# Kernel optimization log

Hardware: AMD Instinct MI355X
Metric: run time of the kernel (lower is better)

Reference implementation:

```python
import jax, jax.numpy as jnp
import numpy as np

TEMPERATURE = 0.07
EPS = 1e-8


def _cosine_sim(a, b):
    # F.cosine_similarity(a[:,None], b[None,:], dim=-1) as a normalized matmul
    an = a / jnp.maximum(jnp.linalg.norm(a, axis=-1, keepdims=True), EPS)
    bn = b / jnp.maximum(jnp.linalg.norm(b, axis=-1, keepdims=True), EPS)
    return an @ bn.T  # [N, M]


def setup_inputs() -> dict:
    key = jax.random.key(0)
    k1, k2, k3, k4 = jax.random.split(key, 4)
    B, M, D, C = 512, 65536, 256, 10
    return {
        "q": jax.random.normal(k1, (B, D), dtype=jnp.float32),
        "labels": jax.random.randint(k2, (B,), 0, C, dtype=jnp.int64),
        "pro_memory": jax.random.normal(k3, (M, D), dtype=jnp.float32),
        "pro_labels": jax.random.randint(k4, (M,), 0, C, dtype=jnp.int64),
    }


def reference(q, labels, pro_memory, pro_labels):
    B = q.shape[0]
    # --- memory branch (adapt_to='prototype'), memory detached ---
    memory_logits = _cosine_sim(q, jax.lax.stop_gradient(pro_memory)) / TEMPERATURE  # [B, M]
    memory_targets = (labels[:, None] == pro_labels[None, :]).astype(jnp.float32)

    # --- source (in-batch) branch; second q is detached in matrix_sim ---
    src_contrast = _cosine_sim(q, jax.lax.stop_gradient(q)) / TEMPERATURE  # [B, B]
    src_max = jax.lax.stop_gradient(jnp.max(src_contrast, axis=1, keepdims=True))
    src_logits = src_contrast - src_max
    src_mask = 1.0 - jnp.eye(B, dtype=jnp.float32)  # zero the diagonal (self)
    src_targets = (labels[:, None] == labels[None, :]).astype(jnp.float32) * src_mask

    targets = jnp.concatenate([src_targets, memory_targets], axis=1)     # [B, B+M]
    logits = jnp.concatenate([src_logits, memory_logits], axis=1)        # [B, B+M]
    exp_logits = jnp.concatenate(
        [jnp.exp(src_logits) * src_mask, jnp.exp(memory_logits)], axis=1
    )
    log_prob = logits - jnp.log(exp_logits.sum(axis=1, keepdims=True))
    mean_log_prob_pos = (targets * log_prob).sum(axis=1) / targets.sum(axis=1)
    return -jnp.mean(mean_log_prob_pos)
```

## Files before the change

kernel.cpp:

```cpp
#include <hip/hip_runtime.h>
#include <stdint.h>
#include <math.h>

#define B_N 512
#define M_N 65536
#define D_N 256
#define C_N 10
#define TEMP_INV 14.285714285714286f
#define LOG2E_F 1.4426950408889634f
#define K2C (LOG2E_F * TEMP_INV)

typedef __attribute__((ext_vector_type(8))) __bf16 bf16x8;
typedef __attribute__((ext_vector_type(4))) float f32x4;

__device__ __forceinline__ unsigned short f2bf(float f) {
  unsigned int u = __float_as_uint(f);
  return (unsigned short)((u + 0x7FFFu + ((u >> 16) & 1u)) >> 16);
}
__device__ __forceinline__ float bf2f(unsigned short s) {
  return __uint_as_float(((unsigned int)s) << 16);
}

__global__ __launch_bounds__(256) void k_norm_full(const float* __restrict__ pm,
                                                   const float* __restrict__ q,
                                                   unsigned short* __restrict__ pnb,
                                                   float* __restrict__ qn,
                                                   unsigned short* __restrict__ qnb,
                                                   unsigned short* __restrict__ qnbF,
                                                   float* __restrict__ P,
                                                   int* __restrict__ cnt,
                                                   float* __restrict__ Zt,
                                                   float* __restrict__ Ss,
                                                   float* __restrict__ ns_,
                                                   float* __restrict__ out) {
  const int tid = threadIdx.x, w = tid >> 6, l = tid & 63;
  const int g = l >> 4, qs = l & 15;
  if (blockIdx.x == 0) {
    for (int i = tid; i < C_N * D_N; i += 256) P[i] = 0.f;
    if (tid < C_N) cnt[tid] = 0;
    for (int i = tid; i < B_N; i += 256) { Zt[i] = 0.f; Ss[i] = 0.f; ns_[i] = 0.f; }
    if (tid == 0) out[0] = 0.f;
  }
  if (blockIdx.x < 2048) {
    const int rbase = blockIdx.x * 32 + w * 8;
#pragma unroll
    for (int it = 0; it < 2; ++it) {
      const int r = rbase + it * 4 + g;
      const float* src = pm + (size_t)r * D_N;
      float4 v[4];
#pragma unroll
      for (int c = 0; c < 4; ++c) v[c] = *(const float4*)(src + qs * 4 + c * 64);
      float ss = 0.f;
#pragma unroll
      for (int c = 0; c < 4; ++c)
        ss += v[c].x * v[c].x + v[c].y * v[c].y + v[c].z * v[c].z + v[c].w * v[c].w;
      ss += __shfl_xor(ss, 1, 64);
      ss += __shfl_xor(ss, 2, 64);
      ss += __shfl_xor(ss, 4, 64);
      ss += __shfl_xor(ss, 8, 64);
      const float rv = 1.0f / fmaxf(sqrtf(ss), 1e-8f);
      unsigned short* dst = pnb + (size_t)r * D_N;
#pragma unroll
      for (int c = 0; c < 4; ++c) {
        ushort4 o;
        o.x = f2bf(v[c].x * rv); o.y = f2bf(v[c].y * rv);
        o.z = f2bf(v[c].z * rv); o.w = f2bf(v[c].w * rv);
        *(ushort4*)(dst + qs * 4 + c * 64) = o;
      }
    }
  } else {
    const int r = (blockIdx.x - 2048) * 16 + w * 4 + g;
    const float* src = q + (size_t)r * D_N;
    float4 v[4];
#pragma unroll
    for (int c = 0; c < 4; ++c) v[c] = *(const float4*)(src + qs * 4 + c * 64);
    float ss = 0.f;
#pragma unroll
    for (int c = 0; c < 4; ++c)
      ss += v[c].x * v[c].x + v[c].y * v[c].y + v[c].z * v[c].z + v[c].w * v[c].w;
    ss += __shfl_xor(ss, 1, 64);
    ss += __shfl_xor(ss, 2, 64);
    ss += __shfl_xor(ss, 4, 64);
    ss += __shfl_xor(ss, 8, 64);
    const float rv = 1.0f / fmaxf(sqrtf(ss), 1e-8f);
    float* dstf = qn + (size_t)r * D_N;
    unsigned short* dstb = qnb + (size_t)r * D_N;
#pragma unroll
    for (int c = 0; c < 4; ++c) {
      float4 o4;
      o4.x = v[c].x * rv; o4.y = v[c].y * rv; o4.z = v[c].z * rv; o4.w = v[c].w * rv;
      *(float4*)(dstf + qs * 4 + c * 64) = o4;
      ushort4 o;
      o.x = f2bf(o4.x); o.y = f2bf(o4.y); o.z = f2bf(o4.z); o.w = f2bf(o4.w);
      *(ushort4*)(dstb + qs * 4 + c * 64) = o;
      const int kc = (qs >> 1) + c * 8;
      *(ushort4*)(qnbF + (((size_t)kc * 512 + r) << 3) + (qs & 1) * 4) = o;
    }
  }
}

__global__ __launch_bounds__(256, 4) void k_mega(const unsigned short* __restrict__ qnb,
                                                 const unsigned short* __restrict__ qnbF,
                                                 const unsigned short* __restrict__ pnb,
                                                 const int* __restrict__ labels,
                                                 const int* __restrict__ pl,
                                                 float* __restrict__ Zt,
                                                 float* __restrict__ Ss,
                                                 float* __restrict__ ns_,
                                                 float* __restrict__ Zpart,
                                                 float* __restrict__ part) {
  __shared__ __align__(16) unsigned char smem[40960];
  const int bid = blockIdx.x;
  const int tid = threadIdx.x, w = tid >> 6, lane = tid & 63;
  const int rsel = lane & 15, hi = lane >> 4;

  if (bid < 1024) {
    unsigned short* Bs = (unsigned short*)smem;
    float* zall = (float*)(smem + 34816);
    const unsigned short* Bb = pnb + (size_t)bid * 64 * D_N;
    {
      bf16x8 t8[8];
#pragma unroll
      for (int i = 0; i < 8; ++i) {
        const int c = i * 256 + tid;
        t8[i] = *(const bf16x8*)(Bb + (size_t)c * 8);
      }
#pragma unroll
      for (int i = 0; i < 8; ++i) {
        const int c = i * 256 + tid;
        const int r = c >> 5, s = c & 31;
        *(bf16x8*)((char*)Bs + r * 544 + s * 16) = t8[i];
      }
    }
    __syncthreads();

#pragma unroll
    for (int bt = 0; bt < 2; ++bt) {
      f32x4 acc[4][4];
#pragma unroll
      for (int mi = 0; mi < 4; ++mi)
#pragma unroll
        for (int ni = 0; ni < 4; ++ni)
          acc[mi][ni] = (f32x4){0.f, 0.f, 0.f, 0.f};
#pragma unroll
      for (int it = 0; it < 8; ++it) {
        const int kc = it * 4 + hi;
        bf16x8 af[4], bfr[4];
#pragma unroll
        for (int mi = 0; mi < 4; ++mi) {
          const int r = bt * 256 + w * 64 + mi * 16 + rsel;
          af[mi] = *(const bf16x8*)(qnbF + (((size_t)kc * 512 + r) << 3));
        }
#pragma unroll
        for (int ni = 0; ni < 4; ++ni) {
          const int rB = ni * 16 + rsel;
          bfr[ni] = *(const bf16x8*)((const char*)Bs + rB * 544 + kc * 16);
        }
#pragma unroll
        for (int mi = 0; mi < 4; ++mi)
#pragma unroll
          for (int ni = 0; ni < 4; ++ni)
            acc[mi][ni] = __builtin_amdgcn_mfma_f32_16x16x32_bf16(af[mi], bfr[ni], acc[mi][ni], 0, 0, 0);
      }
#pragma unroll
      for (int mi = 0; mi < 4; ++mi) {
        float sv[4] = {0.f, 0.f, 0.f, 0.f};
#pragma unroll
        for (int ni = 0; ni < 4; ++ni)
#pragma unroll
          for (int rg = 0; rg < 4; ++rg)
            sv[rg] += __builtin_amdgcn_exp2f(acc[mi][ni][rg] * K2C);
#pragma unroll
        for (int rg = 0; rg < 4; ++rg) {
          float v = sv[rg];
          v += __shfl_xor(v, 1, 64);
          v += __shfl_xor(v, 2, 64);
          v += __shfl_xor(v, 4, 64);
          v += __shfl_xor(v, 8, 64);
          if (rsel == 0)
            zall[bt * 256 + w * 64 + mi * 16 + hi * 4 + rg] = v;
        }
      }
    }
    __syncthreads();
    float* zp = Zpart + (size_t)bid * 512;
    for (int i = tid; i < 512; i += 256) zp[i] = zall[i];
  } else if (bid < 1040) {
    unsigned short* As = (unsigned short*)smem;
    unsigned short* Bs = (unsigned short*)(smem + 16384);
    int* labR = (int*)(smem + 32768);
    int* labJ = (int*)(smem + 33280);
    float* zr = (float*)(smem + 33792);
    float* sr = (float*)(smem + 34304);
    float* nr = (float*)(smem + 34816);
    const int sb_id = bid - 1024;
    const int bt = sb_id >> 2, jt = sb_id & 3;
    const unsigned short* Ab = qnb + (size_t)(bt * 128) * D_N;
    const unsigned short* Bb = qnb + (size_t)(jt * 128) * D_N;
    if (tid < 128) {
      labR[tid] = labels[bt * 128 + tid];
      labJ[tid] = labels[jt * 128 + tid];
      zr[tid] = 0.f; sr[tid] = 0.f; nr[tid] = 0.f;
    }
    f32x4 acc[4][4];
#pragma unroll
    for (int mi = 0; mi < 4; ++mi)
#pragma unroll
      for (int ni = 0; ni < 4; ++ni)
        acc[mi][ni] = (f32x4){0.f, 0.f, 0.f, 0.f};
    const int wr = w >> 1, wc = w & 1;
    for (int ks = 0; ks < 4; ++ks) {
      const int kk = ks * 64;
#pragma unroll
      for (int i = 0; i < 4; ++i) {
        const int cbase = i * 256 + w * 64;
        const int c = cbase + lane;
        const int r = c >> 3;
        const int ss2 = (c & 7) ^ (r & 7);
        __builtin_amdgcn_global_load_lds(
            (const __attribute__((address_space(1))) void*)(Ab + (size_t)r * D_N + kk + ss2 * 8),
            (__attribute__((address_space(3))) void*)(As + cbase * 8), 16, 0, 0);
        __builtin_amdgcn_global_load_lds(
            (const __attribute__((address_space(1))) void*)(Bb + (size_t)r * D_N + kk + ss2 * 8),
            (__attribute__((address_space(3))) void*)(Bs + cbase * 8), 16, 0, 0);
      }
      __syncthreads();
#pragma unroll
      for (int ksl = 0; ksl < 2; ++ksl) {
        const int sb = ksl * 4 + hi;
        bf16x8 af[4], bfr[4];
#pragma unroll
        for (int mi = 0; mi < 4; ++mi) {
          const int r = wr * 64 + mi * 16 + rsel;
          af[mi] = *(const bf16x8*)((const char*)As + r * 128 + ((sb ^ (r & 7)) * 16));
        }
#pragma unroll
        for (int ni = 0; ni < 4; ++ni) {
          const int r = wc * 64 + ni * 16 + rsel;
          bfr[ni] = *(const bf16x8*)((const char*)Bs + r * 128 + ((sb ^ (r & 7)) * 16));
        }
#pragma unroll
        for (int mi = 0; mi < 4; ++mi)
#pragma unroll
          for (int ni = 0; ni < 4; ++ni)
            acc[mi][ni] = __builtin_amdgcn_mfma_f32_16x16x32_bf16(af[mi], bfr[ni], acc[mi][ni], 0, 0, 0);
      }
      __syncthreads();
    }
#pragma unroll
    for (int mi = 0; mi < 4; ++mi) {
      float zs[4] = {0.f, 0.f, 0.f, 0.f};
      float sv[4] = {0.f, 0.f, 0.f, 0.f};
      float nv[4] = {0.f, 0.f, 0.f, 0.f};
#pragma unroll
      for (int ni = 0; ni < 4; ++ni) {
        const int j_loc = wc * 64 + ni * 16 + rsel;
        const int jg = jt * 128 + j_loc;
        const int lj = labJ[j_loc];
#pragma unroll
        for (int rg_ = 0; rg_ < 4; ++rg_) {
          const int r_loc = wr * 64 + mi * 16 + hi * 4 + rg_;
          const int rg = bt * 128 + r_loc;
          const float lg = acc[mi][ni][rg_] * TEMP_INV - TEMP_INV;
          if (rg != jg) {
            zs[rg_] += __builtin_amdgcn_exp2f(lg * LOG2E_F);
            if (labR[r_loc] == lj) { sv[rg_] += lg; nv[rg_] += 1.f; }
          }
        }
      }
#pragma unroll
      for (int rg_ = 0; rg_ < 4; ++rg_) {
        float z = zs[rg_], s = sv[rg_], n = nv[rg_];
        z += __shfl_xor(z, 1, 64); z += __shfl_xor(z, 2, 64);
        z += __shfl_xor(z, 4, 64); z += __shfl_xor(z, 8, 64);
        s += __shfl_xor(s, 1, 64); s += __shfl_xor(s, 2, 64);
        s += __shfl_xor(s, 4, 64); s += __shfl_xor(s, 8, 64);
        n += __shfl_xor(n, 1, 64); n += __shfl_xor(n, 2, 64);
        n += __shfl_xor(n, 4, 64); n += __shfl_xor(n, 8, 64);
        if (rsel == 0) {
          const int r_loc = wr * 64 + mi * 16 + hi * 4 + rg_;
          atomicAdd(&zr[r_loc], z);
          atomicAdd(&sr[r_loc], s);
          atomicAdd(&nr[r_loc], n);
        }
      }
    }
    __syncthreads();
    if (tid < 128) {
      atomicAdd(&Zt[bt * 128 + tid], zr[tid]);
      atomicAdd(&Ss[bt * 128 + tid], sr[tid]);
      atomicAdd(&ns_[bt * 128 + tid], nr[tid]);
    }
  } else {
    const int cb = bid - 1040;
    const int rbase = cb * 128;
    float4 a0 = {0,0,0,0}, a1 = {0,0,0,0}, a2 = {0,0,0,0}, a3 = {0,0,0,0}, a4 = {0,0,0,0};
    float4 a5 = {0,0,0,0}, a6 = {0,0,0,0}, a7 = {0,0,0,0}, a8 = {0,0,0,0}, a9 = {0,0,0,0};
    for (int j = 0; j < 32; ++j) {
      const int row = rbase + j * 4 + w;
      const ushort4 u = *(const ushort4*)(pnb + (size_t)row * D_N + lane * 4);
      float4 v;
      v.x = bf2f(u.x); v.y = bf2f(u.y); v.z = bf2f(u.z); v.w = bf2f(u.w);
      const int cls = pl[row];
      switch (cls) {
        case 0: a0.x += v.x; a0.y += v.y; a0.z += v.z; a0.w += v.w; break;
        case 1: a1.x += v.x; a1.y += v.y; a1.z += v.z; a1.w += v.w; break;
        case 2: a2.x += v.x; a2.y += v.y; a2.z += v.z; a2.w += v.w; break;
        case 3: a3.x += v.x; a3.y += v.y; a3.z += v.z; a3.w += v.w; break;
        case 4: a4.x += v.x; a4.y += v.y; a4.z += v.z; a4.w += v.w; break;
        case 5: a5.x += v.x; a5.y += v.y; a5.z += v.z; a5.w += v.w; break;
        case 6: a6.x += v.x; a6.y += v.y; a6.z += v.z; a6.w += v.w; break;
        case 7: a7.x += v.x; a7.y += v.y; a7.z += v.z; a7.w += v.w; break;
        case 8: a8.x += v.x; a8.y += v.y; a8.z += v.z; a8.w += v.w; break;
        default: a9.x += v.x; a9.y += v.y; a9.z += v.z; a9.w += v.w; break;
      }
    }
    float* Pl = (float*)smem;
#define WRCLS(k, ak) *(float4*)(Pl + ((w * 10 + (k)) * 256 + lane * 4)) = ak;
    WRCLS(0, a0) WRCLS(1, a1) WRCLS(2, a2) WRCLS(3, a3) WRCLS(4, a4)
    WRCLS(5, a5) WRCLS(6, a6) WRCLS(7, a7) WRCLS(8, a8) WRCLS(9, a9)
#undef WRCLS
    __syncthreads();
    float* dst = part + (size_t)cb * (C_N * D_N);
    for (int i = tid; i < C_N * D_N; i += 256)
      dst[i] = Pl[i] + Pl[2560 + i] + Pl[5120 + i] + Pl[7680 + i];
  }
}

__global__ __launch_bounds__(256) void k_reduce2(const float* __restrict__ part,
                                                 const int* __restrict__ pl,
                                                 const float* __restrict__ Zpart,
                                                 float* __restrict__ P,
                                                 int* __restrict__ cnt,
                                                 float* __restrict__ Zt) {
  const int tid = threadIdx.x, w = tid >> 6, lane = tid & 63;
  if (blockIdx.x < 40) {
    __shared__ int xs[4];
    const int c = blockIdx.x >> 2, q = blockIdx.x & 3;
    float s = 0.f;
#pragma unroll 8
    for (int i = 0; i < 128; ++i)
      s += part[(size_t)(q * 128 + i) * (C_N * D_N) + c * 256 + tid];
    atomicAdd(&P[c * 256 + tid], s);
    int x = 0;
    const int* plq = pl + q * 16384;
#pragma unroll 8
    for (int jj = 0; jj < 64; ++jj)
      x += (plq[jj * 256 + tid] == c) ? 1 : 0;
    x += __shfl_xor(x, 32, 64);
    x += __shfl_xor(x, 16, 64);
    x += __shfl_xor(x, 8, 64);
    x += __shfl_xor(x, 4, 64);
    x += __shfl_xor(x, 2, 64);
    x += __shfl_xor(x, 1, 64);
    if (lane == 0) xs[w] = x;
    __syncthreads();
    if (tid == 0) atomicAdd(&cnt[c], xs[0] + xs[1] + xs[2] + xs[3]);
  } else {
    __shared__ float zl[4][64];
    const int zb = blockIdx.x - 40;
    const int b = zb * 64 + (tid & 63);
    const int s = tid >> 6;
    float acc = 0.f;
#pragma unroll 8
    for (int k = 0; k < 256; ++k)
      acc += Zpart[(size_t)(s * 256 + k) * 512 + b];
    zl[s][tid & 63] = acc;
    __syncthreads();
    if (tid < 64)
      Zt[zb * 64 + tid] += zl[0][tid] + zl[1][tid] + zl[2][tid] + zl[3][tid];
  }
}

__global__ __launch_bounds__(256) void k_final(const float* __restrict__ qn,
                                               const int* __restrict__ labels,
                                               const float* __restrict__ P,
                                               const int* __restrict__ cnt,
                                               const float* __restrict__ Zt,
                                               const float* __restrict__ Ss,
                                               const float* __restrict__ ns_,
                                               float* __restrict__ out) {
  __shared__ float partl[4];
  const int tid = threadIdx.x, w = tid >> 6, lane = tid & 63;
  const int b = blockIdx.x * 4 + w;
  const int cls = labels[b];
  const float4 v = *(const float4*)(qn + (size_t)b * D_N + lane * 4);
  const float4 p = *(const float4*)(P + (size_t)cls * D_N + lane * 4);
  float d = v.x * p.x + v.y * p.y + v.z * p.z + v.w * p.w;
  d += __shfl_xor(d, 32, 64);
  d += __shfl_xor(d, 16, 64);
  d += __shfl_xor(d, 8, 64);
  d += __shfl_xor(d, 4, 64);
  d += __shfl_xor(d, 2, 64);
  d += __shfl_xor(d, 1, 64);
  if (lane == 0) {
    const float smem_ = d * TEMP_INV;
    const float ntot = ns_[b] + (float)cnt[cls];
    partl[w] = (Ss[b] + smem_) / ntot - logf(Zt[b]);
  }
  __syncthreads();
  if (tid == 0)
    atomicAdd(out, -(partl[0] + partl[1] + partl[2] + partl[3]) * (1.0f / (float)B_N));
}

extern "C" void kernel_launch(void* const* d_in, const int* in_sizes, int n_in,
                              void* d_out, int out_size, void* d_ws, size_t ws_size,
                              hipStream_t stream) {
  const float* q = (const float*)d_in[0];
  const int* labels = (const int*)d_in[1];
  const float* pm = (const float*)d_in[2];
  const int* pl = (const int*)d_in[3];
  float* out = (float*)d_out;

  char* wsb = (char*)d_ws;
  unsigned short* pnb = (unsigned short*)wsb;
  float* qn = (float*)(wsb + 33554432);
  unsigned short* qnb = (unsigned short*)(wsb + 34078720);
  float* P = (float*)(wsb + 34340864);
  int* cnt = (int*)(wsb + 34351104);
  float* Zt = (float*)(wsb + 34351168);
  float* Ss = (float*)(wsb + 34353216);
  float* ns_ = (float*)(wsb + 34355264);
  float* part = (float*)(wsb + 34357312);
  float* Zpart = (float*)(wsb + 39620672);
  unsigned short* qnbF = (unsigned short*)(wsb + 41717824);

  k_norm_full<<<2080, 256, 0, stream>>>(pm, q, pnb, qn, qnb, qnbF, P, cnt, Zt, Ss, ns_, out);
  k_mega<<<1552, 256, 0, stream>>>(qnb, qnbF, pnb, labels, pl, Zt, Ss, ns_, Zpart, part);
  k_reduce2<<<48, 256, 0, stream>>>(part, pl, Zpart, P, cnt, Zt);
  k_final<<<128, 256, 0, stream>>>(qn, labels, P, cnt, Zt, Ss, ns_, out);
}
```

Measured before the change: 81.08 us.

## Fuse per-class prototype sums into GEMM blocks and retile q fragment layout

The separate 512 class-sum blocks are removed. Each GEMM block now computes per-class column sums from the prototype tile it already holds in shared memory, which avoids re-reading the prototype bank from global memory. The q fragment buffer is reordered so the four k-chunks a lane group needs within one iteration sit next to each other, which should improve load coalescing. The costs are double the partial-sum buffer (1024 rows reduced instead of 512) and a lowered occupancy hint from 4 to 3 blocks, which may change register allocation.

New measurement: 96.87 us. 19.5% more time.

```diff
diff --git a/kernel.cpp b/kernel.cpp
--- a/kernel.cpp
+++ b/kernel.cpp
@@ -94,12 +94,13 @@
       o.x = f2bf(o4.x); o.y = f2bf(o4.y); o.z = f2bf(o4.z); o.w = f2bf(o4.w);
       *(ushort4*)(dstb + qs * 4 + c * 64) = o;
       const int kc = (qs >> 1) + c * 8;
-      *(ushort4*)(qnbF + (((size_t)kc * 512 + r) << 3) + (qs & 1) * 4) = o;
+      const int itc = kc >> 2, hic = kc & 3;
+      *(ushort4*)(qnbF + ((((size_t)itc * 512 + r) * 4 + hic) << 3) + (qs & 1) * 4) = o;
     }
   }
 }
 
-__global__ __launch_bounds__(256, 4) void k_mega(const unsigned short* __restrict__ qnb,
+__global__ __launch_bounds__(256, 3) void k_mega(const unsigned short* __restrict__ qnb,
                                                  const unsigned short* __restrict__ qnbF,
                                                  const unsigned short* __restrict__ pnb,
                                                  const int* __restrict__ labels,
@@ -109,7 +110,7 @@
                                                  float* __restrict__ ns_,
                                                  float* __restrict__ Zpart,
                                                  float* __restrict__ part) {
-  __shared__ __align__(16) unsigned char smem[40960];
+  __shared__ __align__(16) unsigned char smem[37120];
   const int bid = blockIdx.x;
   const int tid = threadIdx.x, w = tid >> 6, lane = tid & 63;
   const int rsel = lane & 15, hi = lane >> 4;
@@ -117,7 +118,9 @@
   if (bid < 1024) {
     unsigned short* Bs = (unsigned short*)smem;
     float* zall = (float*)(smem + 34816);
+    int* plL = (int*)(smem + 36864);
     const unsigned short* Bb = pnb + (size_t)bid * 64 * D_N;
+    if (tid < 64) plL[tid] = pl[bid * 64 + tid];
     {
       bf16x8 t8[8];
 #pragma unroll
@@ -149,7 +152,7 @@
 #pragma unroll
         for (int mi = 0; mi < 4; ++mi) {
           const int r = bt * 256 + w * 64 + mi * 16 + rsel;
-          af[mi] = *(const bf16x8*)(qnbF + (((size_t)kc * 512 + r) << 3));
+          af[mi] = *(const bf16x8*)(qnbF + ((((size_t)it * 512 + r) * 4 + hi) << 3));
         }
 #pragma unroll
         for (int ni = 0; ni < 4; ++ni) {
@@ -185,7 +188,31 @@
     __syncthreads();
     float* zp = Zpart + (size_t)bid * 512;
     for (int i = tid; i < 512; i += 256) zp[i] = zall[i];
-  } else if (bid < 1040) {
+
+    {
+      float s0 = 0.f, s1 = 0.f, s2 = 0.f, s3 = 0.f, s4 = 0.f;
+      float s5 = 0.f, s6 = 0.f, s7 = 0.f, s8 = 0.f, s9 = 0.f;
+#pragma unroll 8
+      for (int r = 0; r < 64; ++r) {
+        const float v = bf2f(*(const unsigned short*)((const char*)Bs + r * 544 + tid * 2));
+        switch (plL[r]) {
+          case 0: s0 += v; break;
+          case 1: s1 += v; break;
+          case 2: s2 += v; break;
+          case 3: s3 += v; break;
+          case 4: s4 += v; break;
+          case 5: s5 += v; break;
+          case 6: s6 += v; break;
+          case 7: s7 += v; break;
+          case 8: s8 += v; break;
+          default: s9 += v; break;
+        }
+      }
+      float* dst = part + (size_t)bid * (C_N * D_N) + tid;
+      dst[0] = s0; dst[256] = s1; dst[512] = s2; dst[768] = s3; dst[1024] = s4;
+      dst[1280] = s5; dst[1536] = s6; dst[1792] = s7; dst[2048] = s8; dst[2304] = s9;
+    }
+  } else {
     unsigned short* As = (unsigned short*)smem;
     unsigned short* Bs = (unsigned short*)(smem + 16384);
     int* labR = (int*)(smem + 32768);
@@ -291,39 +318,6 @@
       atomicAdd(&Ss[bt * 128 + tid], sr[tid]);
       atomicAdd(&ns_[bt * 128 + tid], nr[tid]);
     }
-  } else {
-    const int cb = bid - 1040;
-    const int rbase = cb * 128;
-    float4 a0 = {0,0,0,0}, a1 = {0,0,0,0}, a2 = {0,0,0,0}, a3 = {0,0,0,0}, a4 = {0,0,0,0};
-    float4 a5 = {0,0,0,0}, a6 = {0,0,0,0}, a7 = {0,0,0,0}, a8 = {0,0,0,0}, a9 = {0,0,0,0};
-    for (int j = 0; j < 32; ++j) {
-      const int row = rbase + j * 4 + w;
-      const ushort4 u = *(const ushort4*)(pnb + (size_t)row * D_N + lane * 4);
-      float4 v;
-      v.x = bf2f(u.x); v.y = bf2f(u.y); v.z = bf2f(u.z); v.w = bf2f(u.w);
-      const int cls = pl[row];
-      switch (cls) {
-        case 0: a0.x += v.x; a0.y += v.y; a0.z += v.z; a0.w += v.w; break;
-        case 1: a1.x += v.x; a1.y += v.y; a1.z += v.z; a1.w += v.w; break;
-        case 2: a2.x += v.x; a2.y += v.y; a2.z += v.z; a2.w += v.w; break;
-        case 3: a3.x += v.x; a3.y += v.y; a3.z += v.z; a3.w += v.w; break;
-        case 4: a4.x += v.x; a4.y += v.y; a4.z += v.z; a4.w += v.w; break;
-        case 5: a5.x += v.x; a5.y += v.y; a5.z += v.z; a5.w += v.w; break;
-        case 6: a6.x += v.x; a6.y += v.y; a6.z += v.z; a6.w += v.w; break;
-        case 7: a7.x += v.x; a7.y += v.y; a7.z += v.z; a7.w += v.w; break;
-        case 8: a8.x += v.x; a8.y += v.y; a8.z += v.z; a8.w += v.w; break;
-        default: a9.x += v.x; a9.y += v.y; a9.z += v.z; a9.w += v.w; break;
-      }
-    }
-    float* Pl = (float*)smem;
-#define WRCLS(k, ak) *(float4*)(Pl + ((w * 10 + (k)) * 256 + lane * 4)) = ak;
-    WRCLS(0, a0) WRCLS(1, a1) WRCLS(2, a2) WRCLS(3, a3) WRCLS(4, a4)
-    WRCLS(5, a5) WRCLS(6, a6) WRCLS(7, a7) WRCLS(8, a8) WRCLS(9, a9)
-#undef WRCLS
-    __syncthreads();
-    float* dst = part + (size_t)cb * (C_N * D_N);
-    for (int i = tid; i < C_N * D_N; i += 256)
-      dst[i] = Pl[i] + Pl[2560 + i] + Pl[5120 + i] + Pl[7680 + i];
   }
 }
 
@@ -339,8 +333,8 @@
     const int c = blockIdx.x >> 2, q = blockIdx.x & 3;
     float s = 0.f;
 #pragma unroll 8
-    for (int i = 0; i < 128; ++i)
-      s += part[(size_t)(q * 128 + i) * (C_N * D_N) + c * 256 + tid];
+    for (int i = 0; i < 256; ++i)
+      s += part[(size_t)(q * 256 + i) * (C_N * D_N) + c * 256 + tid];
     atomicAdd(&P[c * 256 + tid], s);
     int x = 0;
     const int* plq = pl + q * 16384;
@@ -422,11 +416,11 @@
   float* Ss = (float*)(wsb + 34353216);
   float* ns_ = (float*)(wsb + 34355264);
   float* part = (float*)(wsb + 34357312);
-  float* Zpart = (float*)(wsb + 39620672);
-  unsigned short* qnbF = (unsigned short*)(wsb + 41717824);
+  float* Zpart = (float*)(wsb + 44843072);
+  unsigned short* qnbF = (unsigned short*)(wsb + 46940224);
 
   k_norm_full<<<2080, 256, 0, stream>>>(pm, q, pnb, qn, qnb, qnbF, P, cnt, Zt, Ss, ns_, out);
-  k_mega<<<1552, 256, 0, stream>>>(qnb, qnbF, pnb, labels, pl, Zt, Ss, ns_, Zpart, part);
+  k_mega<<<1040, 256, 0, stream>>>(qnb, qnbF, pnb, labels, pl, Zt, Ss, ns_, Zpart, part);
   k_reduce2<<<48, 256, 0, stream>>>(part, pl, Zpart, P, cnt, Zt);
   k_final<<<128, 256, 0, stream>>>(qn, labels, P, cnt, Zt, Ss, ns_, out);
 }
```

## Split class-sum work into its own kernel and retile GEMM with 512-thread blocks

Applied to the files above, without the earlier changes.

Moves the per-class prototype accumulation out of the mega kernel into a separate k_class launch. The GEMM kernel now uses 512-thread blocks with 8 waves per 64-row memory tile. Each wave preloads all 16 A fragments for its 32 query rows into registers before the MFMA loop, instead of reloading A fragments from global memory on every k-step. The in-batch GEMM blocks are retiled to 8 waves with 4x2 fragments. The intent is better load balance and more register reuse of the query operand, at the cost of an extra kernel launch, more register pressure, and serialised class-sum work.

Result: slower. 89.48 us (+10.4%).

```diff
diff --git a/kernel.cpp b/kernel.cpp
--- a/kernel.cpp
+++ b/kernel.cpp
@@ -21,18 +21,18 @@
   return __uint_as_float(((unsigned int)s) << 16);
 }
 
-__global__ __launch_bounds__(256) void k_norm_full(const float* __restrict__ pm,
-                                                   const float* __restrict__ q,
-                                                   unsigned short* __restrict__ pnb,
-                                                   float* __restrict__ qn,
-                                                   unsigned short* __restrict__ qnb,
-                                                   unsigned short* __restrict__ qnbF,
-                                                   float* __restrict__ P,
-                                                   int* __restrict__ cnt,
-                                                   float* __restrict__ Zt,
-                                                   float* __restrict__ Ss,
-                                                   float* __restrict__ ns_,
-                                                   float* __restrict__ out) {
+__global__ __launch_bounds__(256) void k_norm(const float* __restrict__ pm,
+                                              const float* __restrict__ q,
+                                              unsigned short* __restrict__ pnb,
+                                              float* __restrict__ qn,
+                                              unsigned short* __restrict__ qnb,
+                                              unsigned short* __restrict__ qnbF,
+                                              float* __restrict__ P,
+                                              int* __restrict__ cnt,
+                                              float* __restrict__ Zt,
+                                              float* __restrict__ Ss,
+                                              float* __restrict__ ns_,
+                                              float* __restrict__ out) {
   const int tid = threadIdx.x, w = tid >> 6, l = tid & 63;
   const int g = l >> 4, qs = l & 15;
   if (blockIdx.x == 0) {
@@ -99,71 +99,107 @@
   }
 }
 
-__global__ __launch_bounds__(256, 4) void k_mega(const unsigned short* __restrict__ qnb,
+__global__ __launch_bounds__(256) void k_class(const unsigned short* __restrict__ pnb,
+                                               const int* __restrict__ pl,
+                                               float* __restrict__ part) {
+  __shared__ float Pl[4 * C_N * D_N];
+  const int tid = threadIdx.x, w = tid >> 6, lane = tid & 63;
+  const int cb = blockIdx.x;
+  const int rbase = cb * 128;
+  float4 a0 = {0,0,0,0}, a1 = {0,0,0,0}, a2 = {0,0,0,0}, a3 = {0,0,0,0}, a4 = {0,0,0,0};
+  float4 a5 = {0,0,0,0}, a6 = {0,0,0,0}, a7 = {0,0,0,0}, a8 = {0,0,0,0}, a9 = {0,0,0,0};
+  for (int j = 0; j < 32; ++j) {
+    const int row = rbase + j * 4 + w;
+    const ushort4 u = *(const ushort4*)(pnb + (size_t)row * D_N + lane * 4);
+    float4 v;
+    v.x = bf2f(u.x); v.y = bf2f(u.y); v.z = bf2f(u.z); v.w = bf2f(u.w);
+    const int cls = pl[row];
+    switch (cls) {
+      case 0: a0.x += v.x; a0.y += v.y; a0.z += v.z; a0.w += v.w; break;
+      case 1: a1.x += v.x; a1.y += v.y; a1.z += v.z; a1.w += v.w; break;
+      case 2: a2.x += v.x; a2.y += v.y; a2.z += v.z; a2.w += v.w; break;
+      case 3: a3.x += v.x; a3.y += v.y; a3.z += v.z; a3.w += v.w; break;
+      case 4: a4.x += v.x; a4.y += v.y; a4.z += v.z; a4.w += v.w; break;
+      case 5: a5.x += v.x; a5.y += v.y; a5.z += v.z; a5.w += v.w; break;
+      case 6: a6.x += v.x; a6.y += v.y; a6.z += v.z; a6.w += v.w; break;
+      case 7: a7.x += v.x; a7.y += v.y; a7.z += v.z; a7.w += v.w; break;
+      case 8: a8.x += v.x; a8.y += v.y; a8.z += v.z; a8.w += v.w; break;
+      default: a9.x += v.x; a9.y += v.y; a9.z += v.z; a9.w += v.w; break;
+    }
+  }
+#define WRCLS(k, ak) *(float4*)(Pl + ((w * 10 + (k)) * 256 + lane * 4)) = ak;
+  WRCLS(0, a0) WRCLS(1, a1) WRCLS(2, a2) WRCLS(3, a3) WRCLS(4, a4)
+  WRCLS(5, a5) WRCLS(6, a6) WRCLS(7, a7) WRCLS(8, a8) WRCLS(9, a9)
+#undef WRCLS
+  __syncthreads();
+  float* dst = part + (size_t)cb * (C_N * D_N);
+  for (int i = tid; i < C_N * D_N; i += 256)
+    dst[i] = Pl[i] + Pl[2560 + i] + Pl[5120 + i] + Pl[7680 + i];
+}
+
+__global__ __launch_bounds__(512, 2) void k_gemm(const unsigned short* __restrict__ pnb,
+                                                 const unsigned short* __restrict__ qnb,
                                                  const unsigned short* __restrict__ qnbF,
-                                                 const unsigned short* __restrict__ pnb,
                                                  const int* __restrict__ labels,
-                                                 const int* __restrict__ pl,
                                                  float* __restrict__ Zt,
                                                  float* __restrict__ Ss,
                                                  float* __restrict__ ns_,
-                                                 float* __restrict__ Zpart,
-                                                 float* __restrict__ part) {
-  __shared__ __align__(16) unsigned char smem[40960];
+                                                 float* __restrict__ Zpart) {
+  __shared__ __align__(16) unsigned char smem[36864];
   const int bid = blockIdx.x;
   const int tid = threadIdx.x, w = tid >> 6, lane = tid & 63;
   const int rsel = lane & 15, hi = lane >> 4;
 
   if (bid < 1024) {
+    const int mt = bid;
     unsigned short* Bs = (unsigned short*)smem;
     float* zall = (float*)(smem + 34816);
-    const unsigned short* Bb = pnb + (size_t)bid * 64 * D_N;
+    const unsigned short* Bb = pnb + (size_t)mt * 64 * D_N;
+    zall[tid] = 0.f;
     {
-      bf16x8 t8[8];
-#pragma unroll
-      for (int i = 0; i < 8; ++i) {
-        const int c = i * 256 + tid;
+      bf16x8 t8[4];
+#pragma unroll
+      for (int i = 0; i < 4; ++i) {
+        const int c = i * 512 + tid;
         t8[i] = *(const bf16x8*)(Bb + (size_t)c * 8);
       }
 #pragma unroll
-      for (int i = 0; i < 8; ++i) {
-        const int c = i * 256 + tid;
+      for (int i = 0; i < 4; ++i) {
+        const int c = i * 512 + tid;
         const int r = c >> 5, s = c & 31;
         *(bf16x8*)((char*)Bs + r * 544 + s * 16) = t8[i];
       }
     }
     __syncthreads();
 
-#pragma unroll
-    for (int bt = 0; bt < 2; ++bt) {
-      f32x4 acc[4][4];
-#pragma unroll
-      for (int mi = 0; mi < 4; ++mi)
-#pragma unroll
-        for (int ni = 0; ni < 4; ++ni)
-          acc[mi][ni] = (f32x4){0.f, 0.f, 0.f, 0.f};
+#pragma unroll 1
+    for (int pass = 0; pass < 2; ++pass) {
+      const int qbase = pass * 256 + w * 32;
+      bf16x8 af[16];
+#pragma unroll
+      for (int t = 0; t < 16; ++t)
+        af[t] = *(const bf16x8*)(qnbF +
+            (((size_t)((t & 7) * 4 + hi) * 512 + qbase + (t >> 3) * 16 + rsel) << 3));
+      __builtin_amdgcn_sched_barrier(0);
+
+      f32x4 acc[2][4];
+#pragma unroll
+      for (int ni = 0; ni < 4; ++ni) {
+        acc[0][ni] = (f32x4){0.f, 0.f, 0.f, 0.f};
+        acc[1][ni] = (f32x4){0.f, 0.f, 0.f, 0.f};
+      }
 #pragma unroll
       for (int it = 0; it < 8; ++it) {
         const int kc = it * 4 + hi;
-        bf16x8 af[4], bfr[4];
-#pragma unroll
-        for (int mi = 0; mi < 4; ++mi) {
-          const int r = bt * 256 + w * 64 + mi * 16 + rsel;
-          af[mi] = *(const bf16x8*)(qnbF + (((size_t)kc * 512 + r) << 3));
-        }
 #pragma unroll
         for (int ni = 0; ni < 4; ++ni) {
-          const int rB = ni * 16 + rsel;
-          bfr[ni] = *(const bf16x8*)((const char*)Bs + rB * 544 + kc * 16);
-        }
-#pragma unroll
-        for (int mi = 0; mi < 4; ++mi)
-#pragma unroll
-          for (int ni = 0; ni < 4; ++ni)
-            acc[mi][ni] = __builtin_amdgcn_mfma_f32_16x16x32_bf16(af[mi], bfr[ni], acc[mi][ni], 0, 0, 0);
-      }
-#pragma unroll
-      for (int mi = 0; mi < 4; ++mi) {
+          const bf16x8 b = *(const bf16x8*)((const char*)Bs + (ni * 16 + rsel) * 544 + kc * 16);
+          acc[0][ni] = __builtin_amdgcn_mfma_f32_16x16x32_bf16(af[it], b, acc[0][ni], 0, 0, 0);
+          acc[1][ni] = __builtin_amdgcn_mfma_f32_16x16x32_bf16(af[8 + it], b, acc[1][ni], 0, 0, 0);
+        }
+      }
+#pragma unroll
+      for (int mi = 0; mi < 2; ++mi) {
         float sv[4] = {0.f, 0.f, 0.f, 0.f};
 #pragma unroll
         for (int ni = 0; ni < 4; ++ni)
@@ -178,42 +214,42 @@
           v += __shfl_xor(v, 4, 64);
           v += __shfl_xor(v, 8, 64);
           if (rsel == 0)
-            zall[bt * 256 + w * 64 + mi * 16 + hi * 4 + rg] = v;
+            zall[qbase + mi * 16 + hi * 4 + rg] = v;
         }
       }
     }
     __syncthreads();
-    float* zp = Zpart + (size_t)bid * 512;
-    for (int i = tid; i < 512; i += 256) zp[i] = zall[i];
-  } else if (bid < 1040) {
+    Zpart[(size_t)mt * 512 + tid] = zall[tid];
+  } else {
     unsigned short* As = (unsigned short*)smem;
-    unsigned short* Bs = (unsigned short*)(smem + 16384);
+    unsigned short* Bs2 = (unsigned short*)(smem + 16384);
     int* labR = (int*)(smem + 32768);
     int* labJ = (int*)(smem + 33280);
     float* zr = (float*)(smem + 33792);
     float* sr = (float*)(smem + 34304);
     float* nr = (float*)(smem + 34816);
     const int sb_id = bid - 1024;
-    const int bt = sb_id >> 2, jt = sb_id & 3;
-    const unsigned short* Ab = qnb + (size_t)(bt * 128) * D_N;
+    const int bt2 = sb_id >> 2, jt = sb_id & 3;
+    const unsigned short* Ab = qnb + (size_t)(bt2 * 128) * D_N;
     const unsigned short* Bb = qnb + (size_t)(jt * 128) * D_N;
     if (tid < 128) {
-      labR[tid] = labels[bt * 128 + tid];
+      labR[tid] = labels[bt2 * 128 + tid];
       labJ[tid] = labels[jt * 128 + tid];
       zr[tid] = 0.f; sr[tid] = 0.f; nr[tid] = 0.f;
     }
-    f32x4 acc[4][4];
+    f32x4 acc[4][2];
 #pragma unroll
     for (int mi = 0; mi < 4; ++mi)
 #pragma unroll
-      for (int ni = 0; ni < 4; ++ni)
+      for (int ni = 0; ni < 2; ++ni)
         acc[mi][ni] = (f32x4){0.f, 0.f, 0.f, 0.f};
-    const int wr = w >> 1, wc = w & 1;
+    const int wr = w >> 2, wc = w & 3;
+#pragma unroll 1
     for (int ks = 0; ks < 4; ++ks) {
       const int kk = ks * 64;
 #pragma unroll
-      for (int i = 0; i < 4; ++i) {
-        const int cbase = i * 256 + w * 64;
+      for (int i = 0; i < 2; ++i) {
+        const int cbase = i * 512 + w * 64;
         const int c = cbase + lane;
         const int r = c >> 3;
         const int ss2 = (c & 7) ^ (r & 7);
@@ -222,27 +258,27 @@
             (__attribute__((address_space(3))) void*)(As + cbase * 8), 16, 0, 0);
         __builtin_amdgcn_global_load_lds(
             (const __attribute__((address_space(1))) void*)(Bb + (size_t)r * D_N + kk + ss2 * 8),
-            (__attribute__((address_space(3))) void*)(Bs + cbase * 8), 16, 0, 0);
+            (__attribute__((address_space(3))) void*)(Bs2 + cbase * 8), 16, 0, 0);
       }
       __syncthreads();
-#pragma unroll
+#pragma unroll 1
       for (int ksl = 0; ksl < 2; ++ksl) {
         const int sb = ksl * 4 + hi;
-        bf16x8 af[4], bfr[4];
+        bf16x8 af[4], bfr[2];
 #pragma unroll
         for (int mi = 0; mi < 4; ++mi) {
           const int r = wr * 64 + mi * 16 + rsel;
           af[mi] = *(const bf16x8*)((const char*)As + r * 128 + ((sb ^ (r & 7)) * 16));
         }
 #pragma unroll
-        for (int ni = 0; ni < 4; ++ni) {
-          const int r = wc * 64 + ni * 16 + rsel;
-          bfr[ni] = *(const bf16x8*)((const char*)Bs + r * 128 + ((sb ^ (r & 7)) * 16));
+        for (int ni = 0; ni < 2; ++ni) {
+          const int r = wc * 32 + ni * 16 + rsel;
+          bfr[ni] = *(const bf16x8*)((const char*)Bs2 + r * 128 + ((sb ^ (r & 7)) * 16));
         }
 #pragma unroll
         for (int mi = 0; mi < 4; ++mi)
 #pragma unroll
-          for (int ni = 0; ni < 4; ++ni)
+          for (int ni = 0; ni < 2; ++ni)
             acc[mi][ni] = __builtin_amdgcn_mfma_f32_16x16x32_bf16(af[mi], bfr[ni], acc[mi][ni], 0, 0, 0);
       }
       __syncthreads();
@@ -253,14 +289,14 @@
       float sv[4] = {0.f, 0.f, 0.f, 0.f};
       float nv[4] = {0.f, 0.f, 0.f, 0.f};
 #pragma unroll
-      for (int ni = 0; ni < 4; ++ni) {
-        const int j_loc = wc * 64 + ni * 16 + rsel;
+      for (int ni = 0; ni < 2; ++ni) {
+        const int j_loc = wc * 32 + ni * 16 + rsel;
         const int jg = jt * 128 + j_loc;
         const int lj = labJ[j_loc];
 #pragma unroll
         for (int rg_ = 0; rg_ < 4; ++rg_) {
           const int r_loc = wr * 64 + mi * 16 + hi * 4 + rg_;
-          const int rg = bt * 128 + r_loc;
+          const int rg = bt2 * 128 + r_loc;
           const float lg = acc[mi][ni][rg_] * TEMP_INV - TEMP_INV;
           if (rg != jg) {
             zs[rg_] += __builtin_amdgcn_exp2f(lg * LOG2E_F);
@@ -287,43 +323,10 @@
     }
     __syncthreads();
     if (tid < 128) {
-      atomicAdd(&Zt[bt * 128 + tid], zr[tid]);
-      atomicAdd(&Ss[bt * 128 + tid], sr[tid]);
-      atomicAdd(&ns_[bt * 128 + tid], nr[tid]);
-    }
-  } else {
-    const int cb = bid - 1040;
-    const int rbase = cb * 128;
-    float4 a0 = {0,0,0,0}, a1 = {0,0,0,0}, a2 = {0,0,0,0}, a3 = {0,0,0,0}, a4 = {0,0,0,0};
-    float4 a5 = {0,0,0,0}, a6 = {0,0,0,0}, a7 = {0,0,0,0}, a8 = {0,0,0,0}, a9 = {0,0,0,0};
-    for (int j = 0; j < 32; ++j) {
-      const int row = rbase + j * 4 + w;
-      const ushort4 u = *(const ushort4*)(pnb + (size_t)row * D_N + lane * 4);
-      float4 v;
-      v.x = bf2f(u.x); v.y = bf2f(u.y); v.z = bf2f(u.z); v.w = bf2f(u.w);
-      const int cls = pl[row];
-      switch (cls) {
-        case 0: a0.x += v.x; a0.y += v.y; a0.z += v.z; a0.w += v.w; break;
-        case 1: a1.x += v.x; a1.y += v.y; a1.z += v.z; a1.w += v.w; break;
-        case 2: a2.x += v.x; a2.y += v.y; a2.z += v.z; a2.w += v.w; break;
-        case 3: a3.x += v.x; a3.y += v.y; a3.z += v.z; a3.w += v.w; break;
-        case 4: a4.x += v.x; a4.y += v.y; a4.z += v.z; a4.w += v.w; break;
-        case 5: a5.x += v.x; a5.y += v.y; a5.z += v.z; a5.w += v.w; break;
-        case 6: a6.x += v.x; a6.y += v.y; a6.z += v.z; a6.w += v.w; break;
-        case 7: a7.x += v.x; a7.y += v.y; a7.z += v.z; a7.w += v.w; break;
-        case 8: a8.x += v.x; a8.y += v.y; a8.z += v.z; a8.w += v.w; break;
-        default: a9.x += v.x; a9.y += v.y; a9.z += v.z; a9.w += v.w; break;
-      }
-    }
-    float* Pl = (float*)smem;
-#define WRCLS(k, ak) *(float4*)(Pl + ((w * 10 + (k)) * 256 + lane * 4)) = ak;
-    WRCLS(0, a0) WRCLS(1, a1) WRCLS(2, a2) WRCLS(3, a3) WRCLS(4, a4)
-    WRCLS(5, a5) WRCLS(6, a6) WRCLS(7, a7) WRCLS(8, a8) WRCLS(9, a9)
-#undef WRCLS
-    __syncthreads();
-    float* dst = part + (size_t)cb * (C_N * D_N);
-    for (int i = tid; i < C_N * D_N; i += 256)
-      dst[i] = Pl[i] + Pl[2560 + i] + Pl[5120 + i] + Pl[7680 + i];
+      atomicAdd(&Zt[bt2 * 128 + tid], zr[tid]);
+      atomicAdd(&Ss[bt2 * 128 + tid], sr[tid]);
+      atomicAdd(&ns_[bt2 * 128 + tid], nr[tid]);
+    }
   }
 }
 
@@ -416,17 +419,18 @@
   unsigned short* pnb = (unsigned short*)wsb;
   float* qn = (float*)(wsb + 33554432);
   unsigned short* qnb = (unsigned short*)(wsb + 34078720);
-  float* P = (float*)(wsb + 34340864);
-  int* cnt = (int*)(wsb + 34351104);
-  float* Zt = (float*)(wsb + 34351168);
-  float* Ss = (float*)(wsb + 34353216);
-  float* ns_ = (float*)(wsb + 34355264);
-  float* part = (float*)(wsb + 34357312);
-  float* Zpart = (float*)(wsb + 39620672);
-  unsigned short* qnbF = (unsigned short*)(wsb + 41717824);
-
-  k_norm_full<<<2080, 256, 0, stream>>>(pm, q, pnb, qn, qnb, qnbF, P, cnt, Zt, Ss, ns_, out);
-  k_mega<<<1552, 256, 0, stream>>>(qnb, qnbF, pnb, labels, pl, Zt, Ss, ns_, Zpart, part);
+  unsigned short* qnbF = (unsigned short*)(wsb + 34340864);
+  float* P = (float*)(wsb + 34603008);
+  int* cnt = (int*)(wsb + 34613248);
+  float* Zt = (float*)(wsb + 34613312);
+  float* Ss = (float*)(wsb + 34615360);
+  float* ns_ = (float*)(wsb + 34617408);
+  float* part = (float*)(wsb + 34619456);
+  float* Zpart = (float*)(wsb + 39862336);
+
+  k_norm<<<2080, 256, 0, stream>>>(pm, q, pnb, qn, qnb, qnbF, P, cnt, Zt, Ss, ns_, out);
+  k_class<<<512, 256, 0, stream>>>(pnb, pl, part);
+  k_gemm<<<1040, 512, 0, stream>>>(pnb, qnb, qnbF, labels, Zt, Ss, ns_, Zpart);
   k_reduce2<<<48, 256, 0, stream>>>(part, pl, Zpart, P, cnt, Zt);
   k_final<<<128, 256, 0, stream>>>(qn, labels, P, cnt, Zt, Ss, ns_, out);
 }
```
